# Performance work log

Hardware: AMD Instinct MI355X
Metric: run time of the kernel (lower is better)

## Reference

```python
import jax, jax.numpy as jnp
import numpy as np
import math

B, T, D = 2, 2048, 512      # batch, n_tp, input_dim
DM, H = 64, 16              # per-head d_model, nhead


def setup_inputs() -> dict:
    key = jax.random.key(0)
    ks = jax.random.split(key, 12)
    s = 0.02
    return {
        "data": jax.random.normal(ks[0], (B, T, D), jnp.float32),
        "mask": jax.random.uniform(ks[1], (B, T, D), jnp.float32),
        "wq": jax.random.normal(ks[2], (D, DM * H), jnp.float32) * s,
        "bq": jnp.zeros((DM * H,), jnp.float32),
        "wk": jax.random.normal(ks[3], (D, DM * H), jnp.float32) * s,
        "bk": jnp.zeros((DM * H,), jnp.float32),
        "wv": jax.random.normal(ks[4], (D, DM * H), jnp.float32) * s,
        "bv": jnp.zeros((DM * H,), jnp.float32),
        "wo": jax.random.normal(ks[5], (DM * H, D), jnp.float32) * s,
        "bo": jnp.zeros((D,), jnp.float32),
    }


def reference(data, mask, wq, bq, wk, bk, wv, bv, wo, bo):
    b, t, d = data.shape
    # NOTE: torch code splits proj as (d_model, nhead): head index is fastest-varying
    def split_heads(x):  # [b,t,DM*H] -> [b,H,t,DM]
        return x.reshape(b, t, DM, H).transpose(0, 3, 1, 2)

    q = split_heads(data @ wq + bq)
    k = split_heads(data @ wk + bk)
    v = split_heads(data @ wv + bv)

    scores = jnp.einsum("bhqd,bhkd->bhqk", q, k) / math.sqrt(DM)
    # padded key positions: rows of mask that sum to exactly 0
    pad = (jnp.sum(mask, axis=-1) == 0.0)  # [b, t] (key axis)
    scores = jnp.where(pad[:, None, None, :], -1e9, scores)
    attn = jax.nn.softmax(scores, axis=-1)  # dropout = identity (eval mode)
    out = jnp.einsum("bhqk,bhkd->bhqd", attn, v)
    # merge as (nhead, d_model) — matches torch permute(0,2,1,3).reshape
    out = out.transpose(0, 2, 1, 3).reshape(b, t, H * DM)
    return out @ wo + bo
```

## Files before the change

### kernel.cpp

```cpp
#include <hip/hip_runtime.h>
#include <hip/hip_bf16.h>

#define B_  2
#define T_  2048
#define D_  512
#define DM_ 64
#define H_  16
#define NQ_ (DM_*H_)
#define NT_ (T_/64)

typedef __bf16 bf16x8 __attribute__((ext_vector_type(8)));
typedef __bf16 bf16x4 __attribute__((ext_vector_type(4)));
typedef float  f32x4  __attribute__((ext_vector_type(4)));
typedef unsigned int u32;

static __device__ __forceinline__ __bf16 bfc(float x) { return (__bf16)x; }
static __device__ __forceinline__ unsigned short f2bf(float x) {
    __bf16 b = (__bf16)x;
    unsigned short u;
    __builtin_memcpy(&u, &b, 2);
    return u;
}
static __device__ __forceinline__ u32 pack2bf(float a, float b) {
    return (u32)f2bf(a) | ((u32)f2bf(b) << 16);
}

#if __has_builtin(__builtin_amdgcn_exp2f)
static __device__ __forceinline__ float EXP2(float x) { return __builtin_amdgcn_exp2f(x); }
#else
static __device__ __forceinline__ float EXP2(float x) {
    float r; asm("v_exp_f32 %0, %1\ns_nop 0" : "=v"(r) : "v"(x)); return r;
}
#endif

#define GLOAD16(gp, lp) \
    __builtin_amdgcn_global_load_lds((const __attribute__((address_space(1))) u32*)(gp), \
                                     (__attribute__((address_space(3))) u32*)(lp), 16, 0, 0)

__global__ __launch_bounds__(256)
void prep_kernel(const float* __restrict__ mask, float* __restrict__ padb,
                 const float* __restrict__ data, unsigned short* __restrict__ dataB,
                 const float* __restrict__ wq, const float* __restrict__ wk,
                 const float* __restrict__ wv, unsigned short* __restrict__ btall,
                 const float* __restrict__ wo, unsigned short* __restrict__ wot)
{
    __shared__ float t[32][33];
    const int bid = blockIdx.x;
    const int tid = threadIdx.x;
    if (bid < 1024) {
        const int row  = bid * 4 + (tid >> 6);
        const int lane = tid & 63;
        const float* p = mask + (size_t)row * D_;
        float4 a = *(const float4*)&p[lane * 8];
        float4 b = *(const float4*)&p[lane * 8 + 4];
        float s = a.x + a.y + a.z + a.w + b.x + b.y + b.z + b.w;
#pragma unroll
        for (int off = 32; off; off >>= 1) s += __shfl_down(s, off);
        if (lane == 0) padb[row] = (s == 0.0f) ? -1e9f : 0.0f;
    } else if (bid < 2048) {
        int i = ((bid - 1024) * 256 + tid) * 8;
        float4 a = *(const float4*)&data[i];
        float4 b = *(const float4*)&data[i + 4];
        bf16x8 u = {bfc(a.x), bfc(a.y), bfc(a.z), bfc(a.w),
                    bfc(b.x), bfc(b.y), bfc(b.z), bfc(b.w)};
        *(bf16x8*)&dataB[i] = u;
    } else if (bid < 3584) {
        const int idx = bid - 2048;
        const int z = idx >> 9, rem = idx & 511;
        const int c0 = (rem & 31) * 32, r0 = (rem >> 5) * 32;
        const float* in = (z == 0) ? wq : (z == 1) ? wk : wv;
        unsigned short* out = btall + (size_t)z * NQ_ * D_;
        const int tx = tid & 31, ty = tid >> 5;
#pragma unroll
        for (int i = 0; i < 4; ++i)
            t[ty * 4 + i][tx] = in[(size_t)(r0 + ty * 4 + i) * NQ_ + c0 + tx];
        __syncthreads();
#pragma unroll
        for (int i = 0; i < 4; ++i) {
            int c  = c0 + ty * 4 + i;
            int rp = (c & 15) * 64 + (c >> 4);
            out[(size_t)rp * D_ + r0 + tx] = f2bf(t[tx][ty * 4 + i]);
        }
    } else {
        const int idx = bid - 3584;
        const int c0 = (idx & 15) * 32, r0 = (idx >> 4) * 32;
        const int tx = tid & 31, ty = tid >> 5;
#pragma unroll
        for (int i = 0; i < 4; ++i)
            t[ty * 4 + i][tx] = wo[(size_t)(r0 + ty * 4 + i) * D_ + c0 + tx];
        __syncthreads();
#pragma unroll
        for (int i = 0; i < 4; ++i)
            wot[(size_t)(c0 + ty * 4 + i) * NQ_ + r0 + tx] = f2bf(t[tx][ty * 4 + i]);
    }
}

__global__ __launch_bounds__(256)
void mgemm_qkv_kernel(const unsigned short* __restrict__ A,
                      const unsigned short* __restrict__ BtAll,
                      const float* __restrict__ bq, const float* __restrict__ bk,
                      const float* __restrict__ bv,
                      unsigned short* __restrict__ Qh, unsigned short* __restrict__ Kh,
                      unsigned short* __restrict__ Vt, float alpha_q)
{
    const int K = D_;
    __shared__ __align__(16) unsigned short Al[2][128 * 64];
    __shared__ __align__(16) unsigned short Bl[2][128 * 64];

    const int tid = threadIdx.x;
    const int w  = tid >> 6, l = tid & 63;
    const int lo = l & 15,  g = l >> 4;
    const int wri = w >> 1, wci = w & 1;
    const int m0 = blockIdx.y * 128, n0 = blockIdx.x * 128;
    const int lrow = l >> 3;
    const int lslot = (l & 7) ^ lrow;

    f32x4 acc[4][4] = {};
    const int nk = K >> 6;

#pragma unroll
    for (int p = 0; p < 4; ++p) {
        int br = w * 32 + p * 8;
        GLOAD16(A     + (size_t)(m0 + br + lrow) * K + lslot * 8, (char*)Al[0] + br * 128);
        GLOAD16(BtAll + (size_t)(n0 + br + lrow) * K + lslot * 8, (char*)Bl[0] + br * 128);
    }
    __syncthreads();

    for (int t = 0; t < nk; ++t) {
        const int cur = t & 1;
        if (t + 1 < nk) {
            const int k0 = (t + 1) << 6;
#pragma unroll
            for (int p = 0; p < 4; ++p) {
                int br = w * 32 + p * 8;
                GLOAD16(A     + (size_t)(m0 + br + lrow) * K + k0 + lslot * 8,
                        (char*)Al[cur ^ 1] + br * 128);
                GLOAD16(BtAll + (size_t)(n0 + br + lrow) * K + k0 + lslot * 8,
                        (char*)Bl[cur ^ 1] + br * 128);
            }
        }
#pragma unroll
        for (int kk = 0; kk < 2; ++kk) {
            bf16x8 af[4], bfr[4];
#pragma unroll
            for (int i = 0; i < 4; ++i) {
                int row = wri * 64 + i * 16 + lo;
                af[i] = *(const bf16x8*)&Al[cur][row * 64 + ((((kk << 2) + g) ^ (row & 7)) << 3)];
                int col = wci * 64 + i * 16 + lo;
                bfr[i] = *(const bf16x8*)&Bl[cur][col * 64 + ((((kk << 2) + g) ^ (col & 7)) << 3)];
            }
#pragma unroll
            for (int i = 0; i < 4; ++i)
#pragma unroll
                for (int j = 0; j < 4; ++j)
                    acc[i][j] = __builtin_amdgcn_mfma_f32_16x16x32_bf16(af[i], bfr[j], acc[i][j], 0, 0, 0);
        }
        __syncthreads();
    }

    const int seg = n0 >> 10;
    const int n0l = n0 & 1023;
    const float* bias = (seg == 0) ? bq : (seg == 1) ? bk : bv;
    const float alpha = (seg == 0) ? alpha_q : 1.0f;
    const int h = (n0l >> 6) + wci;

    float bb[4];
#pragma unroll
    for (int j = 0; j < 4; ++j) bb[j] = bias[(j * 16 + lo) * 16 + h];

    const int mb_l = wri * 64 + g * 4;
    if (seg < 2) {
        unsigned short* o16 = (seg == 0) ? Qh : Kh;
        unsigned short* hb = (unsigned short*)Al + wci * (128 * 64);
#pragma unroll
        for (int i = 0; i < 4; ++i)
#pragma unroll
            for (int jj = 0; jj < 4; ++jj) {
                int ml = mb_l + i * 16 + jj;
#pragma unroll
                for (int j = 0; j < 4; ++j) {
                    int dm = j * 16 + lo;
                    int off = ml * 64 + (((dm >> 3) ^ (ml & 7)) << 3) + (dm & 7);
                    hb[off] = f2bf((acc[i][j][jj] + bb[j]) * alpha);
                }
            }
        __syncthreads();
        const int rrow = l >> 3, rch = l & 7;
#pragma unroll
        for (int p = 0; p < 8; ++p) {
            int ml = wri * 64 + p * 8 + rrow;
            bf16x8 v = *(const bf16x8*)&hb[ml * 64 + (((rch ^ (ml & 7))) << 3)];
            int m = m0 + ml;
            int t = m & (T_ - 1), bidx = m >> 11;
            *(bf16x8*)&o16[(((size_t)(bidx * H_ + h)) * T_ + t) * DM_ + rch * 8] = v;
        }
    } else {
#pragma unroll
        for (int i = 0; i < 4; ++i)
#pragma unroll
            for (int j = 0; j < 4; ++j) {
                int m = m0 + mb_l + i * 16;
                int t = m & (T_ - 1), bidx = m >> 11;
                int dm = j * 16 + lo;
                bf16x4 u = {bfc(acc[i][j][0] + bb[j]), bfc(acc[i][j][1] + bb[j]),
                            bfc(acc[i][j][2] + bb[j]), bfc(acc[i][j][3] + bb[j])};
                *(bf16x4*)&Vt[((size_t)(bidx * H_ + h) * DM_ + dm) * T_ + t] = u;
            }
    }
}

__global__ __launch_bounds__(256)
void mgemm_out_kernel(const unsigned short* __restrict__ A,
                      const unsigned short* __restrict__ Bt,
                      const float* __restrict__ bias, float* __restrict__ out,
                      int M, int N, int K)
{
    __shared__ __align__(16) unsigned short Al[2][64 * 64];
    __shared__ __align__(16) unsigned short Bl[2][128 * 64];

    const int tid = threadIdx.x;
    const int w  = tid >> 6, l = tid & 63;
    const int lo = l & 15,  g = l >> 4;
    const int wri = w >> 1, wci = w & 1;
    const int m0 = blockIdx.y * 64, n0 = blockIdx.x * 128;
    const int lrow = l >> 3;
    const int lslot = (l & 7) ^ lrow;

    f32x4 acc[2][4] = {};
    const int nk = K >> 6;

#pragma unroll
    for (int p = 0; p < 2; ++p) {
        int br = w * 16 + p * 8;
        GLOAD16(A + (size_t)(m0 + br + lrow) * K + lslot * 8, (char*)Al[0] + br * 128);
    }
#pragma unroll
    for (int p = 0; p < 4; ++p) {
        int br = w * 32 + p * 8;
        GLOAD16(Bt + (size_t)(n0 + br + lrow) * K + lslot * 8, (char*)Bl[0] + br * 128);
    }
    __syncthreads();

    for (int t = 0; t < nk; ++t) {
        const int cur = t & 1;
        if (t + 1 < nk) {
            const int k0 = (t + 1) << 6;
#pragma unroll
            for (int p = 0; p < 2; ++p) {
                int br = w * 16 + p * 8;
                GLOAD16(A + (size_t)(m0 + br + lrow) * K + k0 + lslot * 8,
                        (char*)Al[cur ^ 1] + br * 128);
            }
#pragma unroll
            for (int p = 0; p < 4; ++p) {
                int br = w * 32 + p * 8;
                GLOAD16(Bt + (size_t)(n0 + br + lrow) * K + k0 + lslot * 8,
                        (char*)Bl[cur ^ 1] + br * 128);
            }
        }
#pragma unroll
        for (int kk = 0; kk < 2; ++kk) {
            bf16x8 af[2], bfr[4];
#pragma unroll
            for (int i = 0; i < 2; ++i) {
                int row = wri * 32 + i * 16 + lo;
                af[i] = *(const bf16x8*)&Al[cur][row * 64 + ((((kk << 2) + g) ^ (row & 7)) << 3)];
            }
#pragma unroll
            for (int j = 0; j < 4; ++j) {
                int col = wci * 64 + j * 16 + lo;
                bfr[j] = *(const bf16x8*)&Bl[cur][col * 64 + ((((kk << 2) + g) ^ (col & 7)) << 3)];
            }
#pragma unroll
            for (int i = 0; i < 2; ++i)
#pragma unroll
                for (int j = 0; j < 4; ++j)
                    acc[i][j] = __builtin_amdgcn_mfma_f32_16x16x32_bf16(af[i], bfr[j], acc[i][j], 0, 0, 0);
        }
        __syncthreads();
    }

    const int mb = m0 + wri * 32 + g * 4;
#pragma unroll
    for (int j = 0; j < 4; ++j) {
        int n = n0 + wci * 64 + j * 16 + lo;
        float bb = bias[n];
#pragma unroll
        for (int i = 0; i < 2; ++i)
#pragma unroll
            for (int jj = 0; jj < 4; ++jj) {
                int m = mb + i * 16 + jj;
                out[(size_t)m * N + n] = acc[i][j][jj] + bb;
            }
    }
}

__global__ __launch_bounds__(128, 2)
void attn_kernel(const unsigned short* __restrict__ Qh,
                 const unsigned short* __restrict__ Kh,
                 const unsigned short* __restrict__ Vt,
                 const float* __restrict__ padb,
                 unsigned short* __restrict__ ctx)
{
    __shared__ __align__(16) unsigned short Ks[2][64 * 64];
    __shared__ __align__(16) unsigned short Vs[2][64 * 64];
    __shared__ __align__(16) float pbs[T_];

    const int tid  = threadIdx.x;
    const int w    = tid >> 6;
    const int l    = tid & 63;
    const int lo16 = l & 15;
    const int g    = l >> 4;
    const int lrow = l >> 3;
    const int lslot = (l & 7) ^ lrow;

    const int f   = blockIdx.x;
    const int s   = f >> 3;
    const int bh  = (f & 7) * 4 + (s >> 5);
    const int q0  = (s & 31) * 64;
    const int bb  = bh >> 4;
    const int hh  = bh & 15;

    bf16x8 qf[2][2];
#pragma unroll
    for (int qt = 0; qt < 2; ++qt) {
        const unsigned short* Qp =
            Qh + ((size_t)bh * T_ + q0 + w * 32 + qt * 16 + lo16) * DM_ + g * 8;
        qf[qt][0] = *(const bf16x8*)(Qp);
        qf[qt][1] = *(const bf16x8*)(Qp + 32);
    }

    const unsigned short* kgp =
        Kh + (size_t)bh * T_ * DM_ + (size_t)(w * 32 + lrow) * DM_ + lslot * 8;
    const unsigned short* vgp =
        Vt + (size_t)bh * DM_ * T_ + (size_t)(w * 32 + lrow) * T_ + lslot * 8;

    {
        const float* src = padb + bb * T_ + tid * 16;
#pragma unroll
        for (int i = 0; i < 4; ++i)
            *(float4*)&pbs[tid * 16 + i * 4] = *(const float4*)(src + i * 4);
    }

#pragma unroll
    for (int p = 0; p < 4; ++p) {
        GLOAD16(kgp + p * 8 * DM_, (char*)Ks[0] + (w * 32 + p * 8) * 128);
        GLOAD16(vgp + p * 8 * T_,  (char*)Vs[0] + (w * 32 + p * 8) * 128);
    }
    kgp += 64 * DM_;
    vgp += 64;
    __syncthreads();

    f32x4 oa[2][4] = {};
    f32x4 ls4[2] = {};

    char* Kr = (char*)Ks[0]; char* Kw = (char*)Ks[1];
    char* Vr = (char*)Vs[0]; char* Vw = (char*)Vs[1];

    for (int t = 0; t < NT_; ++t) {
        if (t + 1 < NT_) {
#pragma unroll
            for (int p = 0; p < 4; ++p) {
                GLOAD16(kgp + p * 8 * DM_, Kw + (w * 32 + p * 8) * 128);
                GLOAD16(vgp + p * 8 * T_,  Vw + (w * 32 + p * 8) * 128);
            }
            kgp += 64 * DM_;
            vgp += 64;
        }

        f32x4 sa[2][4];
#pragma unroll
        for (int nt = 0; nt < 4; ++nt) {
            f32x4 pb4 = *(const f32x4*)&pbs[t * 64 + nt * 16 + g * 4];
            sa[0][nt] = pb4;
            sa[1][nt] = pb4;
        }
        __builtin_amdgcn_s_setprio(1);
#pragma unroll
        for (int ks = 0; ks < 2; ++ks) {
#pragma unroll
            for (int nt = 0; nt < 4; ++nt) {
                int row = nt * 16 + lo16;
                int off = (row * 128 + ks * 64 + g * 16) ^ ((row & 7) << 4);
                bf16x8 kf = *(const bf16x8*)(Kr + off);
#pragma unroll
                for (int qt = 0; qt < 2; ++qt)
                    sa[qt][nt] = __builtin_amdgcn_mfma_f32_16x16x32_bf16(kf, qf[qt][ks], sa[qt][nt], 0, 0, 0);
            }
        }
        __builtin_amdgcn_s_setprio(0);

        u32 pw[2][4][2];
#pragma unroll
        for (int qt = 0; qt < 2; ++qt)
#pragma unroll
            for (int nt = 0; nt < 4; ++nt) {
                float e0 = EXP2(sa[qt][nt][0]);
                float e1 = EXP2(sa[qt][nt][1]);
                float e2 = EXP2(sa[qt][nt][2]);
                float e3 = EXP2(sa[qt][nt][3]);
                ls4[qt] += (f32x4){e0, e1, e2, e3};
                pw[qt][nt][0] = pack2bf(e0, e1);
                pw[qt][nt][1] = pack2bf(e2, e3);
            }
        bf16x8 pf[2][2];
#pragma unroll
        for (int qt = 0; qt < 2; ++qt)
#pragma unroll
            for (int ks = 0; ks < 2; ++ks) {
                uint4 uu;
                uu.x = pw[qt][2 * ks][0];
                uu.y = pw[qt][2 * ks][1];
                uu.z = pw[qt][2 * ks + 1][0];
                uu.w = pw[qt][2 * ks + 1][1];
                pf[qt][ks] = *(const bf16x8*)&uu;
            }

        __builtin_amdgcn_s_setprio(1);
#pragma unroll
        for (int ks = 0; ks < 2; ++ks)
#pragma unroll
            for (int nd = 0; nd < 4; ++nd) {
                int row = nd * 16 + lo16;
                int sw = (row & 7) << 4;
                int o0 = (row * 128 + ks * 64 + g * 8) ^ sw;
                int o1 = (row * 128 + ks * 64 + 32 + g * 8) ^ sw;
                uint2 a = *(const uint2*)(Vr + o0);
                uint2 b = *(const uint2*)(Vr + o1);
                uint4 uu; uu.x = a.x; uu.y = a.y; uu.z = b.x; uu.w = b.y;
                bf16x8 vf = *(const bf16x8*)&uu;
#pragma unroll
                for (int qt = 0; qt < 2; ++qt)
                    oa[qt][nd] = __builtin_amdgcn_mfma_f32_16x16x32_bf16(vf, pf[qt][ks], oa[qt][nd], 0, 0, 0);
            }
        __builtin_amdgcn_s_setprio(0);

        __syncthreads();
        { char* t0 = Kr; Kr = Kw; Kw = t0;
          char* t1 = Vr; Vr = Vw; Vw = t1; }
    }

#pragma unroll
    for (int qt = 0; qt < 2; ++qt) {
        float lt = (ls4[qt][0] + ls4[qt][1]) + (ls4[qt][2] + ls4[qt][3]);
        lt += __shfl_xor(lt, 16);
        lt += __shfl_xor(lt, 32);
        float linv = 1.0f / lt;
        const size_t crow =
            ((size_t)(bb * T_ + q0 + w * 32 + qt * 16 + lo16)) * NQ_ + hh * DM_;
#pragma unroll
        for (int nd = 0; nd < 4; ++nd) {
            bf16x4 u = {bfc(oa[qt][nd][0] * linv), bfc(oa[qt][nd][1] * linv),
                        bfc(oa[qt][nd][2] * linv), bfc(oa[qt][nd][3] * linv)};
            *(bf16x4*)&ctx[crow + nd * 16 + g * 4] = u;
        }
    }
}

extern "C" void kernel_launch(void* const* d_in, const int* in_sizes, int n_in,
                              void* d_out, int out_size, void* d_ws, size_t ws_size,
                              hipStream_t stream) {
    const float* data = (const float*)d_in[0];
    const float* mask = (const float*)d_in[1];
    const float* wq   = (const float*)d_in[2];
    const float* bq   = (const float*)d_in[3];
    const float* wk   = (const float*)d_in[4];
    const float* bk   = (const float*)d_in[5];
    const float* wv   = (const float*)d_in[6];
    const float* bv   = (const float*)d_in[7];
    const float* wo   = (const float*)d_in[8];
    const float* bo   = (const float*)d_in[9];
    float* out = (float*)d_out;

    char* ws = (char*)d_ws;
    const size_t MB = 1024 * 1024;
    unsigned short* Qh    = (unsigned short*)(ws);
    unsigned short* Kh    = (unsigned short*)(ws +  8 * MB);
    unsigned short* Vt    = (unsigned short*)(ws + 16 * MB);
    unsigned short* CTX   = (unsigned short*)(ws + 24 * MB);
    unsigned short* dataB = (unsigned short*)(ws + 32 * MB);
    unsigned short* BtAll = (unsigned short*)(ws + 36 * MB);
    unsigned short* wot   = (unsigned short*)(ws + 39 * MB);
    float*          padb  = (float*)         (ws + 40 * MB);

    const int M = B_ * T_;
    const float alpha_q = 0.125f * 1.44269504089f;

    prep_kernel<<<4096, 256, 0, stream>>>(mask, padb, data, dataB,
                                          wq, wk, wv, BtAll, wo, wot);

    mgemm_qkv_kernel<<<dim3(3 * NQ_ / 128, M / 128), 256, 0, stream>>>(
        dataB, BtAll, bq, bk, bv, Qh, Kh, Vt, alpha_q);

    attn_kernel<<<1024, 128, 0, stream>>>(Qh, Kh, Vt, padb, CTX);

    mgemm_out_kernel<<<dim3(D_ / 128, M / 64), 256, 0, stream>>>(
        CTX, wot, bo, out, M, D_, NQ_);
}
```

Baseline: 100.9 us.

## Triple-buffer K/V tiles and widen attention blocks to 128 queries

```diff
diff --git a/kernel.cpp b/kernel.cpp
--- a/kernel.cpp
+++ b/kernel.cpp
@@ -295,15 +295,15 @@
     }
 }
 
-__global__ __launch_bounds__(128, 2)
+__global__ __launch_bounds__(256, 2)
 void attn_kernel(const unsigned short* __restrict__ Qh,
                  const unsigned short* __restrict__ Kh,
                  const unsigned short* __restrict__ Vt,
                  const float* __restrict__ padb,
                  unsigned short* __restrict__ ctx)
 {
-    __shared__ __align__(16) unsigned short Ks[2][64 * 64];
-    __shared__ __align__(16) unsigned short Vs[2][64 * 64];
+    __shared__ __align__(16) unsigned short Ks[3][64 * 64];
+    __shared__ __align__(16) unsigned short Vs[3][64 * 64];
     __shared__ __align__(16) float pbs[T_];
 
     const int tid  = threadIdx.x;
@@ -316,8 +316,8 @@
 
     const int f   = blockIdx.x;
     const int s   = f >> 3;
-    const int bh  = (f & 7) * 4 + (s >> 5);
-    const int q0  = (s & 31) * 64;
+    const int bh  = (f & 7) * 4 + (s >> 4);
+    const int q0  = (s & 15) * 128;
     const int bb  = bh >> 4;
     const int hh  = bh & 15;
 
@@ -331,39 +331,46 @@
     }
 
     const unsigned short* kgp =
-        Kh + (size_t)bh * T_ * DM_ + (size_t)(w * 32 + lrow) * DM_ + lslot * 8;
+        Kh + (size_t)bh * T_ * DM_ + (size_t)(w * 16 + lrow) * DM_ + lslot * 8;
     const unsigned short* vgp =
-        Vt + (size_t)bh * DM_ * T_ + (size_t)(w * 32 + lrow) * T_ + lslot * 8;
+        Vt + (size_t)bh * DM_ * T_ + (size_t)(w * 16 + lrow) * T_ + lslot * 8;
 
     {
-        const float* src = padb + bb * T_ + tid * 16;
-#pragma unroll
-        for (int i = 0; i < 4; ++i)
-            *(float4*)&pbs[tid * 16 + i * 4] = *(const float4*)(src + i * 4);
-    }
-
-#pragma unroll
-    for (int p = 0; p < 4; ++p) {
-        GLOAD16(kgp + p * 8 * DM_, (char*)Ks[0] + (w * 32 + p * 8) * 128);
-        GLOAD16(vgp + p * 8 * T_,  (char*)Vs[0] + (w * 32 + p * 8) * 128);
-    }
-    kgp += 64 * DM_;
-    vgp += 64;
-    __syncthreads();
+        const float* src = padb + bb * T_ + tid * 8;
+        float4 a = *(const float4*)(src);
+        float4 b = *(const float4*)(src + 4);
+        *(float4*)&pbs[tid * 8]     = a;
+        *(float4*)&pbs[tid * 8 + 4] = b;
+    }
+
+    GLOAD16(kgp,           (char*)Ks[0] + (w * 16) * 128);
+    GLOAD16(kgp + 8 * DM_, (char*)Ks[0] + (w * 16 + 8) * 128);
+    GLOAD16(vgp,           (char*)Vs[0] + (w * 16) * 128);
+    GLOAD16(vgp + 8 * T_,  (char*)Vs[0] + (w * 16 + 8) * 128);
+    kgp += 64 * DM_; vgp += 64;
+    GLOAD16(kgp,           (char*)Ks[1] + (w * 16) * 128);
+    GLOAD16(kgp + 8 * DM_, (char*)Ks[1] + (w * 16 + 8) * 128);
+    GLOAD16(vgp,           (char*)Vs[1] + (w * 16) * 128);
+    GLOAD16(vgp + 8 * T_,  (char*)Vs[1] + (w * 16 + 8) * 128);
+    kgp += 64 * DM_; vgp += 64;
+
+    asm volatile("s_waitcnt vmcnt(4)" ::: "memory");
+    __builtin_amdgcn_sched_barrier(0);
+    __builtin_amdgcn_s_barrier();
 
     f32x4 oa[2][4] = {};
     f32x4 ls4[2] = {};
 
-    char* Kr = (char*)Ks[0]; char* Kw = (char*)Ks[1];
-    char* Vr = (char*)Vs[0]; char* Vw = (char*)Vs[1];
+    char* Kr = (char*)Ks[0]; char* Kn = (char*)Ks[1]; char* Kw = (char*)Ks[2];
+    char* Vr = (char*)Vs[0]; char* Vn = (char*)Vs[1]; char* Vw = (char*)Vs[2];
 
     for (int t = 0; t < NT_; ++t) {
-        if (t + 1 < NT_) {
-#pragma unroll
-            for (int p = 0; p < 4; ++p) {
-                GLOAD16(kgp + p * 8 * DM_, Kw + (w * 32 + p * 8) * 128);
-                GLOAD16(vgp + p * 8 * T_,  Vw + (w * 32 + p * 8) * 128);
-            }
+        const bool more2 = (t + 2 < NT_);
+        if (more2) {
+            GLOAD16(kgp,           Kw + (w * 16) * 128);
+            GLOAD16(kgp + 8 * DM_, Kw + (w * 16 + 8) * 128);
+            GLOAD16(vgp,           Vw + (w * 16) * 128);
+            GLOAD16(vgp + 8 * T_,  Vw + (w * 16 + 8) * 128);
             kgp += 64 * DM_;
             vgp += 64;
         }
@@ -435,9 +442,18 @@
             }
         __builtin_amdgcn_s_setprio(0);
 
-        __syncthreads();
-        { char* t0 = Kr; Kr = Kw; Kw = t0;
-          char* t1 = Vr; Vr = Vw; Vw = t1; }
+        if (t + 1 < NT_) {
+            if (more2) {
+                asm volatile("s_waitcnt vmcnt(4)" ::: "memory");
+            } else {
+                asm volatile("s_waitcnt vmcnt(0)" ::: "memory");
+            }
+            __builtin_amdgcn_sched_barrier(0);
+            __builtin_amdgcn_s_barrier();
+        }
+
+        { char* tk = Kr; Kr = Kn; Kn = Kw; Kw = tk;
+          char* tv = Vr; Vr = Vn; Vn = Vw; Vw = tv; }
     }
 
 #pragma unroll
@@ -492,7 +508,7 @@
     mgemm_qkv_kernel<<<dim3(3 * NQ_ / 128, M / 128), 256, 0, stream>>>(
         dataB, BtAll, bq, bk, bv, Qh, Kh, Vt, alpha_q);
 
-    attn_kernel<<<1024, 128, 0, stream>>>(Qh, Kh, Vt, padb, CTX);
+    attn_kernel<<<512, 256, 0, stream>>>(Qh, Kh, Vt, padb, CTX);
 
     mgemm_out_kernel<<<dim3(D_ / 128, M / 64), 256, 0, stream>>>(
         CTX, wot, bo, out, M, D_, NQ_);
```

New measurement: 97.54 us. -3.3%, faster.
